# Kernel optimization log

Hardware: AMD Instinct MI355X
Metric: run time of the kernel (lower is better)

The kernel has to match this reference:

```python
import jax, jax.numpy as jnp
import numpy as np

N, H, W, C = 2048, 64, 64, 8
E, G, M = 4, 512, 512            # experts, group size per class, max_output_cells
CELLS = [128, 256, 384, 512]     # classes_config.values()


def setup_inputs() -> dict:
    key = jax.random.key(0)
    k = jax.random.split(key, 6)
    inputs = jax.random.normal(k[0], (N, H, W, C), dtype=jnp.float32)
    # input_config: class -> sample indices (equal partition of the batch)
    indices = jnp.arange(N, dtype=jnp.int32).reshape(E, G)
    W1 = jax.random.normal(k[1], (E, 1, 1, C, C), dtype=jnp.float32) * 0.1
    W3 = jax.random.normal(k[2], (E, 3, 3, C, C), dtype=jnp.float32) * 0.1
    Wskip = jax.random.normal(k[3], (E, 1, 1, C, 2 * C), dtype=jnp.float32) * 0.1
    Wd = jax.random.normal(k[4], (E, 2 * C, M), dtype=jnp.float32) * 0.1
    # zero-pad each expert's output beyond its num_output_layer_cells
    cell_mask = (jnp.arange(M)[None, :] < jnp.asarray(CELLS)[:, None]).astype(jnp.float32)
    return {"inputs": inputs, "indices": indices, "W1": W1, "W3": W3,
            "Wskip": Wskip, "Wd": Wd, "cell_mask": cell_mask}


def _conv(x, w):
    # x: [G,H,W,Cin], w: [kh,kw,Cin,Cout] -> [G,H,W,Cout], SAME padding
    return jax.lax.conv_general_dilated(x, w, (1, 1), 'SAME',
                                        dimension_numbers=('NHWC', 'HWIO', 'NHWC'))


def _expert(x, w1, w3, ws, wd, mask):
    # Hybrid inception + skip: parallel 1x1/3x3 branches, channel concat, 1x1-projected skip
    b1 = jax.nn.relu(_conv(x, w1))           # [G,H,W,C]
    b2 = jax.nn.relu(_conv(x, w3))           # [G,H,W,C]
    y = jnp.concatenate([b1, b2], axis=-1) + _conv(x, ws)  # [G,H,W,2C]
    pooled = y.mean(axis=(1, 2))             # [G,2C]
    return (pooled @ wd) * mask[None, :]     # [G,M], padded to max_output_cells


def reference(inputs, indices, W1, W3, Wskip, Wd, cell_mask):
    # class-indexed gather: [E,G,H,W,C]
    groups = inputs[indices]
    # dispatch each group to its expert, vmapped over experts
    outs = jax.vmap(_expert)(groups, W1, W3, Wskip, Wd, cell_mask)  # [E,G,M]
    # concat along batch in class order (matches outputs.extend + tf.concat axis=0)
    return outs.reshape(E * G, M)
```

## Files before the change

kernel.cpp:

```cpp
#include <hip/hip_runtime.h>
#include <hip/hip_bf16.h>

#define MM 512
#define ROWSZ (66 * 8)

typedef short bf16x8 __attribute__((ext_vector_type(8)));
typedef float f32x4  __attribute__((ext_vector_type(4)));

static __device__ inline short f2bf(float f) {
    __hip_bfloat16 h = __float2bfloat16(f);
    return *reinterpret_cast<short*>(&h);
}

__global__ __launch_bounds__(256, 4)
void conv_moe_mfma(const float* __restrict__ x,
                   const int*   __restrict__ idx,
                   const float* __restrict__ W1,
                   const float* __restrict__ W3,
                   const float* __restrict__ Wsk,
                   const float* __restrict__ Wd,
                   const float* __restrict__ cmask,
                   float*       __restrict__ out)
{
    __shared__ short xbf[18][66][8];
    __shared__ float red[4][16];
    __shared__ float redx[4][8];
    __shared__ float rsum[16];
    __shared__ float rsumx[8];
    __shared__ float pooledS[16];

    const int b    = blockIdx.x;
    const int e    = b >> 9;
    const int tid  = threadIdx.x;
    const int lane = tid & 63;
    const int wid  = tid >> 6;
    const int g    = lane >> 4;
    const int p    = lane & 15;
    const int CB   = wid << 4;

    const int samp = idx[b];
    const float* xb = x + (size_t)samp * 32768;

    const float* w3 = W3 + e * 576;
    const float* w1 = W1 + e * 64;
    bf16x8 bf0, bf1, bf2, bid;
    #pragma unroll
    for (int j = 0; j < 8; ++j) {
        float v0 = 0.f, v1 = 0.f, v2 = 0.f, vi = 0.f;
        if (p >= 8) {
            v0 = w3[g * 64 + j * 8 + (p - 8)];
            v1 = w3[(4 + g) * 64 + j * 8 + (p - 8)];
            if (g == 0) v2 = w3[8 * 64 + j * 8 + (p - 8)];
        } else {
            if (g == 0) { v1 = w1[j * 8 + p]; vi = (j == p) ? 1.f : 0.f; }
        }
        bf0[j] = f2bf(v0); bf1[j] = f2bf(v1); bf2[j] = f2bf(v2); bid[j] = f2bf(vi);
    }

    int off0, off1, off2;
    { const int t = g;     const int dr = t / 3, dc = t % 3; off0 = (dr * 66 + CB + p + dc) * 8; }
    { const int t = 4 + g; const int dr = t / 3, dc = t % 3; off1 = (dr * 66 + CB + p + dc) * 8; }
    {                      const int dr = 2,     dc = 2;     off2 = (dr * 66 + CB + p + dc) * 8; }

    if (tid < 36) {
        const int rr = tid >> 1, side = tid & 1;
        bf16x8 zv = {0,0,0,0,0,0,0,0};
        *(bf16x8*)&xbf[rr][side ? 65 : 0][0] = zv;
    }

    const float4 z4 = make_float4(0.f, 0.f, 0.f, 0.f);
    float4 ra[5][2];

    #pragma unroll
    for (int j5 = 0; j5 < 5; ++j5) {
        const int j = j5 * 256 + tid;
        ra[j5][0] = z4; ra[j5][1] = z4;
        if (j < 1152) {
            const int lrow = j >> 6, c = j & 63;
            const int r = lrow - 1;
            if (r >= 0) {
                const float4* s4 = (const float4*)(xb + (((r << 6) + c) << 3));
                ra[j5][0] = s4[0];
                ra[j5][1] = s4[1];
            }
        }
    }
    #pragma unroll
    for (int j5 = 0; j5 < 5; ++j5) {
        const int j = j5 * 256 + tid;
        if (j < 1152) {
            const int lrow = j >> 6, c = j & 63;
            bf16x8 v;
            v[0] = f2bf(ra[j5][0].x); v[1] = f2bf(ra[j5][0].y);
            v[2] = f2bf(ra[j5][0].z); v[3] = f2bf(ra[j5][0].w);
            v[4] = f2bf(ra[j5][1].x); v[5] = f2bf(ra[j5][1].y);
            v[6] = f2bf(ra[j5][1].z); v[7] = f2bf(ra[j5][1].w);
            *(bf16x8*)&xbf[lrow][c + 1][0] = v;
        }
    }
    __syncthreads();

    f32x4 ssum = {0.f, 0.f, 0.f, 0.f};
    f32x4 acc2 = {0.f, 0.f, 0.f, 0.f};

    #pragma unroll 1
    for (int s = 0; s < 4; ++s) {
        if (s < 3) {
            const int rbase = 16 * (s + 1) + 1;
            #pragma unroll
            for (int j5 = 0; j5 < 4; ++j5) {
                const int j = j5 * 256 + tid;
                const int lrow = j >> 6, c = j & 63;
                const int r = rbase + lrow;
                ra[j5][0] = z4; ra[j5][1] = z4;
                if (r < 64) {
                    const float4* s4 = (const float4*)(xb + (((r << 6) + c) << 3));
                    ra[j5][0] = s4[0];
                    ra[j5][1] = s4[1];
                }
            }
        }

        {
            const short* base = &xbf[0][0][0];
            #pragma unroll 2
            for (int rl = 0; rl < 16; ++rl) {
                const short* rbase2 = base + rl * ROWSZ;
                const bf16x8 a0 = *(const bf16x8*)(rbase2 + off0);
                const bf16x8 a1 = *(const bf16x8*)(rbase2 + off1);
                const bf16x8 a2 = *(const bf16x8*)(rbase2 + off2);
                f32x4 d = {0.f, 0.f, 0.f, 0.f};
                d = __builtin_amdgcn_mfma_f32_16x16x32_bf16(a0, bf0, d, 0, 0, 0);
                d = __builtin_amdgcn_mfma_f32_16x16x32_bf16(a1, bf1, d, 0, 0, 0);
                d = __builtin_amdgcn_mfma_f32_16x16x32_bf16(a2, bf2, d, 0, 0, 0);
                acc2 = __builtin_amdgcn_mfma_f32_16x16x32_bf16(a1, bid, acc2, 0, 0, 0);
                ssum[0] += fmaxf(d[0], 0.f);
                ssum[1] += fmaxf(d[1], 0.f);
                ssum[2] += fmaxf(d[2], 0.f);
                ssum[3] += fmaxf(d[3], 0.f);
            }
        }

        bf16x8 rcopy;
        if (s < 3 && tid < 128)
            rcopy = *(const bf16x8*)&xbf[16 + (tid >> 6)][(tid & 63) + 1][0];

        __syncthreads();

        if (s < 3) {
            if (tid < 128)
                *(bf16x8*)&xbf[tid >> 6][(tid & 63) + 1][0] = rcopy;
            #pragma unroll
            for (int j5 = 0; j5 < 4; ++j5) {
                const int j = j5 * 256 + tid;
                const int lrow = 2 + (j >> 6), c = j & 63;
                bf16x8 v;
                v[0] = f2bf(ra[j5][0].x); v[1] = f2bf(ra[j5][0].y);
                v[2] = f2bf(ra[j5][0].z); v[3] = f2bf(ra[j5][0].w);
                v[4] = f2bf(ra[j5][1].x); v[5] = f2bf(ra[j5][1].y);
                v[6] = f2bf(ra[j5][1].z); v[7] = f2bf(ra[j5][1].w);
                *(bf16x8*)&xbf[lrow][c + 1][0] = v;
            }
            __syncthreads();
        }
    }

    float scon = ssum[0] + ssum[1] + ssum[2] + ssum[3];
    float sxs  = acc2[0] + acc2[1] + acc2[2] + acc2[3];
    scon += __shfl_xor(scon, 16);
    scon += __shfl_xor(scon, 32);
    sxs  += __shfl_xor(sxs, 16);
    sxs  += __shfl_xor(sxs, 32);
    if (lane < 16) red[wid][lane]  = scon;
    if (lane < 8)  redx[wid][lane] = sxs;
    __syncthreads();
    if (tid < 16) rsum[tid]  = (red[0][tid] + red[1][tid] + red[2][tid] + red[3][tid]) * (1.f / 4096.f);
    if (tid < 8)  rsumx[tid] = (redx[0][tid] + redx[1][tid] + redx[2][tid] + redx[3][tid]) * (1.f / 4096.f);
    __syncthreads();

    if (tid < 16) {
        float acc = rsum[tid];
        #pragma unroll
        for (int ci = 0; ci < 8; ++ci)
            acc += rsumx[ci] * Wsk[e * 128 + ci * 16 + tid];
        pooledS[tid] = acc;
    }
    __syncthreads();

    const float* wd = Wd + (size_t)e * 16 * MM;
    const float* cm = cmask + e * MM;
    #pragma unroll 1
    for (int m = tid; m < MM; m += 256) {
        float acc = 0.f;
        #pragma unroll
        for (int k = 0; k < 16; ++k) acc += pooledS[k] * wd[k * MM + m];
        out[(size_t)b * MM + m] = acc * cm[m];
    }
}

extern "C" void kernel_launch(void* const* d_in, const int* in_sizes, int n_in,
                              void* d_out, int out_size, void* d_ws, size_t ws_size,
                              hipStream_t stream) {
    const float* x    = (const float*)d_in[0];
    const int*   idx  = (const int*)  d_in[1];
    const float* W1   = (const float*)d_in[2];
    const float* W3   = (const float*)d_in[3];
    const float* Wsk  = (const float*)d_in[4];
    const float* Wd   = (const float*)d_in[5];
    const float* cmsk = (const float*)d_in[6];
    float* out = (float*)d_out;

    conv_moe_mfma<<<2048, 256, 0, stream>>>(x, idx, W1, W3, Wsk, Wd, cmsk, out);
}
```

Baseline: 52.30 us.

## Reorganize 3x3 conv MFMA into row-sliding A fragments; compute skip sum in fp32

Remaps the 3x3 conv so each lane group covers one kernel column and all three kernel rows become three MFMAs whose A operands slide down the row. Each iteration then loads one new LDS fragment instead of three. The identity MFMA that summed input channels for the skip path is removed; input sums are now accumulated in fp32 registers during staging and reduced with wavefront shuffles. This cuts LDS reads and MFMA count per row, at the cost of extra VALU adds and 48 shuffles in the epilogue, and the inner loop is now fully unrolled.

```diff
diff --git a/kernel.cpp b/kernel.cpp
--- a/kernel.cpp
+++ b/kernel.cpp
@@ -43,24 +43,24 @@
 
     const float* w3 = W3 + e * 576;
     const float* w1 = W1 + e * 64;
-    bf16x8 bf0, bf1, bf2, bid;
+    bf16x8 B0, B1, B2;
     #pragma unroll
     for (int j = 0; j < 8; ++j) {
-        float v0 = 0.f, v1 = 0.f, v2 = 0.f, vi = 0.f;
-        if (p >= 8) {
-            v0 = w3[g * 64 + j * 8 + (p - 8)];
-            v1 = w3[(4 + g) * 64 + j * 8 + (p - 8)];
-            if (g == 0) v2 = w3[8 * 64 + j * 8 + (p - 8)];
-        } else {
-            if (g == 0) { v1 = w1[j * 8 + p]; vi = (j == p) ? 1.f : 0.f; }
-        }
-        bf0[j] = f2bf(v0); bf1[j] = f2bf(v1); bf2[j] = f2bf(v2); bid[j] = f2bf(vi);
-    }
-
-    int off0, off1, off2;
-    { const int t = g;     const int dr = t / 3, dc = t % 3; off0 = (dr * 66 + CB + p + dc) * 8; }
-    { const int t = 4 + g; const int dr = t / 3, dc = t % 3; off1 = (dr * 66 + CB + p + dc) * 8; }
-    {                      const int dr = 2,     dc = 2;     off2 = (dr * 66 + CB + p + dc) * 8; }
+        float v0 = 0.f, v1 = 0.f, v2 = 0.f;
+        if (g < 3) {
+            if (p >= 8) {
+                v0 = w3[(0 * 3 + g) * 64 + j * 8 + (p - 8)];
+                v1 = w3[(1 * 3 + g) * 64 + j * 8 + (p - 8)];
+                v2 = w3[(2 * 3 + g) * 64 + j * 8 + (p - 8)];
+            } else if (g == 1) {
+                v1 = w1[j * 8 + p];
+            }
+        }
+        B0[j] = f2bf(v0); B1[j] = f2bf(v1); B2[j] = f2bf(v2);
+    }
+
+    const int gi  = (g < 3) ? g : 2;
+    const int offA = (CB + p + gi) * 8;
 
     if (tid < 36) {
         const int rr = tid >> 1, side = tid & 1;
@@ -70,6 +70,7 @@
 
     const float4 z4 = make_float4(0.f, 0.f, 0.f, 0.f);
     float4 ra[5][2];
+    float4 sxa = z4, sxb = z4;
 
     #pragma unroll
     for (int j5 = 0; j5 < 5; ++j5) {
@@ -90,6 +91,10 @@
         const int j = j5 * 256 + tid;
         if (j < 1152) {
             const int lrow = j >> 6, c = j & 63;
+            sxa.x += ra[j5][0].x; sxa.y += ra[j5][0].y;
+            sxa.z += ra[j5][0].z; sxa.w += ra[j5][0].w;
+            sxb.x += ra[j5][1].x; sxb.y += ra[j5][1].y;
+            sxb.z += ra[j5][1].z; sxb.w += ra[j5][1].w;
             bf16x8 v;
             v[0] = f2bf(ra[j5][0].x); v[1] = f2bf(ra[j5][0].y);
             v[2] = f2bf(ra[j5][0].z); v[3] = f2bf(ra[j5][0].w);
@@ -101,7 +106,6 @@
     __syncthreads();
 
     f32x4 ssum = {0.f, 0.f, 0.f, 0.f};
-    f32x4 acc2 = {0.f, 0.f, 0.f, 0.f};
 
     #pragma unroll 1
     for (int s = 0; s < 4; ++s) {
@@ -122,22 +126,23 @@
         }
 
         {
-            const short* base = &xbf[0][0][0];
-            #pragma unroll 2
+            const short* base = &xbf[0][0][0] + offA;
+            bf16x8 A0 = *(const bf16x8*)(base + 0 * ROWSZ);
+            bf16x8 A1 = *(const bf16x8*)(base + 1 * ROWSZ);
+            bf16x8 A2 = *(const bf16x8*)(base + 2 * ROWSZ);
+            #pragma unroll
             for (int rl = 0; rl < 16; ++rl) {
-                const short* rbase2 = base + rl * ROWSZ;
-                const bf16x8 a0 = *(const bf16x8*)(rbase2 + off0);
-                const bf16x8 a1 = *(const bf16x8*)(rbase2 + off1);
-                const bf16x8 a2 = *(const bf16x8*)(rbase2 + off2);
+                bf16x8 A3 = A2;
+                if (rl < 15) A3 = *(const bf16x8*)(base + (rl + 3) * ROWSZ);
                 f32x4 d = {0.f, 0.f, 0.f, 0.f};
-                d = __builtin_amdgcn_mfma_f32_16x16x32_bf16(a0, bf0, d, 0, 0, 0);
-                d = __builtin_amdgcn_mfma_f32_16x16x32_bf16(a1, bf1, d, 0, 0, 0);
-                d = __builtin_amdgcn_mfma_f32_16x16x32_bf16(a2, bf2, d, 0, 0, 0);
-                acc2 = __builtin_amdgcn_mfma_f32_16x16x32_bf16(a1, bid, acc2, 0, 0, 0);
+                d = __builtin_amdgcn_mfma_f32_16x16x32_bf16(A0, B0, d, 0, 0, 0);
+                d = __builtin_amdgcn_mfma_f32_16x16x32_bf16(A1, B1, d, 0, 0, 0);
+                d = __builtin_amdgcn_mfma_f32_16x16x32_bf16(A2, B2, d, 0, 0, 0);
                 ssum[0] += fmaxf(d[0], 0.f);
                 ssum[1] += fmaxf(d[1], 0.f);
                 ssum[2] += fmaxf(d[2], 0.f);
                 ssum[3] += fmaxf(d[3], 0.f);
+                A0 = A1; A1 = A2; A2 = A3;
             }
         }
 
@@ -154,6 +159,10 @@
             for (int j5 = 0; j5 < 4; ++j5) {
                 const int j = j5 * 256 + tid;
                 const int lrow = 2 + (j >> 6), c = j & 63;
+                sxa.x += ra[j5][0].x; sxa.y += ra[j5][0].y;
+                sxa.z += ra[j5][0].z; sxa.w += ra[j5][0].w;
+                sxb.x += ra[j5][1].x; sxb.y += ra[j5][1].y;
+                sxb.z += ra[j5][1].z; sxb.w += ra[j5][1].w;
                 bf16x8 v;
                 v[0] = f2bf(ra[j5][0].x); v[1] = f2bf(ra[j5][0].y);
                 v[2] = f2bf(ra[j5][0].z); v[3] = f2bf(ra[j5][0].w);
@@ -166,14 +175,21 @@
     }
 
     float scon = ssum[0] + ssum[1] + ssum[2] + ssum[3];
-    float sxs  = acc2[0] + acc2[1] + acc2[2] + acc2[3];
     scon += __shfl_xor(scon, 16);
     scon += __shfl_xor(scon, 32);
-    sxs  += __shfl_xor(sxs, 16);
-    sxs  += __shfl_xor(sxs, 32);
-    if (lane < 16) red[wid][lane]  = scon;
-    if (lane < 8)  redx[wid][lane] = sxs;
-    __syncthreads();
+    if (lane < 16) red[wid][lane] = scon;
+
+    float sxv[8] = {sxa.x, sxa.y, sxa.z, sxa.w, sxb.x, sxb.y, sxb.z, sxb.w};
+    #pragma unroll
+    for (int i = 0; i < 8; ++i)
+        #pragma unroll
+        for (int off = 32; off > 0; off >>= 1)
+            sxv[i] += __shfl_xor(sxv[i], off);
+    if (lane == 0)
+        #pragma unroll
+        for (int i = 0; i < 8; ++i) redx[wid][i] = sxv[i];
+    __syncthreads();
+
     if (tid < 16) rsum[tid]  = (red[0][tid] + red[1][tid] + red[2][tid] + red[3][tid]) * (1.f / 4096.f);
     if (tid < 8)  rsumx[tid] = (redx[0][tid] + redx[1][tid] + redx[2][tid] + redx[3][tid]) * (1.f / 4096.f);
     __syncthreads();
```

Result: slower. 114.7 us (+119.4%).
